# Kernel tuning notes

Measured on AMD Instinct MI355X. Metric: run time of the kernel, lower is better.

Reference implementation:

```python
import jax, jax.numpy as jnp
import numpy as np

N_NODES = 100000
N_EDGES = 1600000
IN_CH = 128
HID = 128   # 2 * out_channels
OUT = 64


def setup_inputs() -> dict:
    key = jax.random.key(0)
    ks = jax.random.split(key, 6)
    x = jax.random.normal(ks[0], (N_NODES, IN_CH), dtype=jnp.float32)
    edge_index = jax.random.randint(ks[1], (2, N_EDGES), 0, N_NODES, dtype=jnp.int64)
    # Glorot-ish scaled weights
    W1 = jax.random.normal(ks[2], (IN_CH, HID), dtype=jnp.float32) * (1.0 / np.sqrt(IN_CH))
    b1 = jnp.zeros((HID,), dtype=jnp.float32)
    Wmu = jax.random.normal(ks[3], (HID, OUT), dtype=jnp.float32) * (1.0 / np.sqrt(HID))
    bmu = jnp.zeros((OUT,), dtype=jnp.float32)
    Wlv = jax.random.normal(ks[4], (HID, OUT), dtype=jnp.float32) * (1.0 / np.sqrt(HID))
    blv = jnp.zeros((OUT,), dtype=jnp.float32)
    return {"x": x, "edge_index": edge_index, "W1": W1, "b1": b1,
            "Wmu": Wmu, "bmu": bmu, "Wlv": Wlv, "blv": blv}


def reference(x, edge_index, W1, b1, Wmu, bmu, Wlv, blv):
    n = x.shape[0]
    loops = jnp.arange(n, dtype=edge_index.dtype)
    src = jnp.concatenate([edge_index[0], loops])  # [E + N]
    dst = jnp.concatenate([edge_index[1], loops])
    # GCN symmetric normalization with self-loops (cached=True -> compute once, reuse)
    deg = jax.ops.segment_sum(jnp.ones_like(src, dtype=x.dtype), dst, num_segments=n)
    dinv = jnp.where(deg > 0, jax.lax.rsqrt(jnp.maximum(deg, 1.0)), 0.0)
    norm = (dinv[src] * dinv[dst])[:, None]  # [E+N, 1]

    def gcn(h, W, b):
        h = h @ W                              # dense transform first (smaller gather width)
        msg = h[src] * norm                    # gather + edge scaling
        return jax.ops.segment_sum(msg, dst, num_segments=n) + b

    h = jax.nn.relu(gcn(x, W1, b1))
    mu = gcn(h, Wmu, bmu)
    logvar = gcn(h, Wlv, blv)
    return (mu, logvar)
```

## Files before the change

kernel.cpp:

```cpp
#include <hip/hip_runtime.h>
#include <hip/hip_fp16.h>


using half8 = __attribute__((ext_vector_type(8))) _Float16;
using f32x4 = __attribute__((ext_vector_type(4))) float;
using f32x2 = __attribute__((ext_vector_type(2))) float;

constexpr int CAP = 8192;

__global__ void detect_kernel(const int* __restrict__ ei, int* __restrict__ mode) {
    int lane = threadIdx.x & 63;
    int any = 0;
    for (int k = lane; k < 1024; k += 64) any |= ei[2 * k + 1];
    unsigned long long b = __ballot(any != 0);
    if (threadIdx.x == 0) *mode = (b == 0ull) ? 1 : 0;
}

__global__ __launch_bounds__(256) void partition_kernel(
    const int* __restrict__ ei, int E, int n, const int* __restrict__ mode,
    int* __restrict__ bcnt, unsigned* __restrict__ pairs) {
    __shared__ int hist[512];
    __shared__ int base[512];
    int t = threadIdx.x;
    for (int i = t; i < 512; i += 256) hist[i] = 0;
    __syncthreads();
    int m = *mode;
    int e0 = blockIdx.x * 4096;
    int s_[16], d_[16], o_[16];
#pragma unroll
    for (int k = 0; k < 16; ++k) {
        int e = e0 + k * 256 + t;
        d_[k] = -1;
        if (e < E) {
            int s = m ? ei[2 * e] : ei[e];
            int d = m ? ei[2 * (E + e)] : ei[E + e];
            if ((unsigned)d < (unsigned)n && (unsigned)s < (unsigned)n) {
                s_[k] = s;
                d_[k] = d;
                o_[k] = atomicAdd(&hist[d >> 8], 1);
            }
        }
    }
    __syncthreads();
    int K = (n + 255) >> 8;
    for (int b = t; b < K; b += 256) {
        int h = hist[b];
        base[b] = h ? atomicAdd(&bcnt[b], h) : 0;
    }
    __syncthreads();
#pragma unroll
    for (int k = 0; k < 16; ++k) {
        if (d_[k] >= 0) {
            int b = d_[k] >> 8;
            unsigned p = (unsigned)s_[k] | ((unsigned)(d_[k] & 255) << 24);
            pairs[(size_t)b * CAP + base[b] + o_[k]] = p;
        }
    }
}

__global__ __launch_bounds__(256) void build_kernel(
    const unsigned* __restrict__ pairs, const int* __restrict__ bcnt,
    int2* __restrict__ rowbe, float* __restrict__ dinv,
    int* __restrict__ csr_src, int n) {
    __shared__ int hist[256];
    __shared__ int wtot[4];
    int b = blockIdx.x;
    int cnt = bcnt[b];
    size_t gbase = (size_t)b * CAP;
    int tid = threadIdx.x, lane = tid & 63, wv = tid >> 6;
    hist[tid] = 0;
    __syncthreads();
    for (int i = tid; i < cnt; i += 256)
        atomicAdd(&hist[pairs[gbase + i] >> 24], 1);
    __syncthreads();
    int v = hist[tid];
    int incl = v;
#pragma unroll
    for (int off = 1; off < 64; off <<= 1) {
        int t = __shfl_up(incl, off, 64);
        if (lane >= off) incl += t;
    }
    if (lane == 63) wtot[wv] = incl;
    __syncthreads();
    int wo = 0;
    for (int w = 0; w < wv; ++w) wo += wtot[w];
    int ex = wo + incl - v;
    int node = (b << 8) + tid;
    if (node < n) {
        int beg = (int)gbase + ex;
        rowbe[node] = make_int2(beg, beg + v);
        dinv[node] = rsqrtf((float)(v + 1));
    }
    __syncthreads();
    hist[tid] = ex;
    __syncthreads();
    for (int i = tid; i < cnt; i += 256) {
        unsigned p = pairs[gbase + i];
        int pos = atomicAdd(&hist[p >> 24], 1);
        csr_src[gbase + pos] = (int)(p & 0x00FFFFFFu);
    }
}

template <int MODE>
__global__ __launch_bounds__(256) void agg_row_kernel(
    const __half* __restrict__ T, const float* __restrict__ dinv,
    const int2* __restrict__ rowbe, const int* __restrict__ csr_src,
    const float* __restrict__ biasa, const float* __restrict__ biasb,
    void* __restrict__ outa, void* __restrict__ outb, int n) {
    int wave = (int)((blockIdx.x * blockDim.x + threadIdx.x) >> 6);
    int lane = threadIdx.x & 63;
    if (wave >= n) return;
    const __half2* x2 = (const __half2*)T;
    float di = dinv[wave];
    float2 xf = __half22float2(x2[((size_t)wave << 6) + lane]);
    float ax = 0.f, ay = 0.f;
    int2 be = rowbe[wave];
    int e = be.x, end = be.y;
    for (; e + 8 <= end; e += 8) {
        int s[8];
        float w[8];
        float2 u[8];
#pragma unroll
        for (int k = 0; k < 8; ++k)
            s[k] = __builtin_amdgcn_readfirstlane(csr_src[e + k]);
#pragma unroll
        for (int k = 0; k < 8; ++k) w[k] = dinv[s[k]];
#pragma unroll
        for (int k = 0; k < 8; ++k)
            u[k] = __half22float2(x2[((size_t)s[k] << 6) + lane]);
#pragma unroll
        for (int k = 0; k < 8; ++k) {
            ax += w[k] * u[k].x;
            ay += w[k] * u[k].y;
        }
    }
    for (; e < end; ++e) {
        int s = __builtin_amdgcn_readfirstlane(csr_src[e]);
        float w = dinv[s];
        float2 u = __half22float2(x2[((size_t)s << 6) + lane]);
        ax += w * u.x;
        ay += w * u.y;
    }
    const float* bp = (lane < 32) ? biasa : biasb;
    float2 bv = *(const float2*)(bp + ((2 * lane) & 63));
    float vx = di * (di * xf.x + ax) + bv.x;
    float vy = di * (di * xf.y + ay) + bv.y;
    if (MODE == 0) {
        vx = fmaxf(vx, 0.f);
        vy = fmaxf(vy, 0.f);
        __half2 hv = __floats2half2_rn(vx, vy);
        unsigned int bits;
        __builtin_memcpy(&bits, &hv, 4);
        unsigned int* o = (unsigned int*)outa;
        __builtin_nontemporal_store(bits, o + ((size_t)wave << 6) + lane);
    } else {
        float* o = (lane < 32) ? (float*)outa : (float*)outb;
        int cc = (2 * lane) & 63;
        f32x2 v = {vx, vy};
        __builtin_nontemporal_store(v, (f32x2*)(o + (size_t)wave * 64 + cc));
    }
}

__global__ void packw_kernel(const float* __restrict__ Wa,
                             const float* __restrict__ Wb,
                             __half* __restrict__ dst) {
    int t = blockIdx.x * 256 + threadIdx.x;
    int lane = t & 63;
    int fk = t >> 6;
    int kt = fk & 3, nt = fk >> 2;
    int k0 = kt * 32 + ((lane >> 4) << 3);
    int c = nt * 16 + (lane & 15);
    const float* W;
    int ldw, cc;
    if (Wb) {
        W = (c < 64) ? Wa : Wb;
        cc = c & 63;
        ldw = 64;
    } else {
        W = Wa;
        cc = c;
        ldw = 128;
    }
    __half tmp[8];
#pragma unroll
    for (int e = 0; e < 8; ++e)
        tmp[e] = __float2half(W[(size_t)(k0 + e) * ldw + cc]);
    *(float4*)(dst + (size_t)t * 8) = *(float4*)tmp;
}

template <typename AT>
__global__ __launch_bounds__(256) void gemm_pure_kernel(
    const AT* __restrict__ A, const __half* __restrict__ Wp,
    __half* __restrict__ outh, int n) {
    int lane = threadIdx.x & 63;
    int wv = threadIdx.x >> 6;
    int m0 = (blockIdx.x * 4 + wv) * 16;
    if (m0 >= n) return;
    int row_a = m0 + (lane & 15);
    if (row_a >= n) row_a = n - 1;
    half8 afr[4];
    if constexpr (sizeof(AT) == 4) {
        const float4* Arow = (const float4*)(A + (size_t)row_a * 128);
#pragma unroll
        for (int kt = 0; kt < 4; ++kt) {
            float4 lo = Arow[kt * 8 + ((lane >> 4) << 1)];
            float4 hi = Arow[kt * 8 + ((lane >> 4) << 1) + 1];
            half8 h;
            h[0] = (_Float16)lo.x; h[1] = (_Float16)lo.y;
            h[2] = (_Float16)lo.z; h[3] = (_Float16)lo.w;
            h[4] = (_Float16)hi.x; h[5] = (_Float16)hi.y;
            h[6] = (_Float16)hi.z; h[7] = (_Float16)hi.w;
            afr[kt] = h;
        }
    } else {
        const half8* Arow = (const half8*)(A + (size_t)row_a * 128);
#pragma unroll
        for (int kt = 0; kt < 4; ++kt) afr[kt] = Arow[kt * 4 + (lane >> 4)];
    }

    const half8* Wf = (const half8*)Wp;
    int colw = lane & 15;
    int rbase = m0 + ((lane >> 4) << 2);

#pragma unroll
    for (int nt = 0; nt < 8; ++nt) {
        f32x4 acc = {0.f, 0.f, 0.f, 0.f};
#pragma unroll
        for (int kt = 0; kt < 4; ++kt)
            acc = __builtin_amdgcn_mfma_f32_16x16x32_f16(
                afr[kt], Wf[(nt * 4 + kt) * 64 + lane], acc, 0, 0, 0);
        int c = nt * 16 + colw;
#pragma unroll
        for (int e = 0; e < 4; ++e) {
            int r = rbase + e;
            if (r < n) outh[(size_t)r * 128 + c] = __float2half(acc[e]);
        }
    }
}

extern "C" void kernel_launch(void* const* d_in, const int* in_sizes, int n_in,
                              void* d_out, int out_size, void* d_ws, size_t ws_size,
                              hipStream_t stream) {
    const float* x   = (const float*)d_in[0];
    const int*   ei  = (const int*)d_in[1];
    const float* W1  = (const float*)d_in[2];
    const float* b1  = (const float*)d_in[3];
    const float* Wmu = (const float*)d_in[4];
    const float* bmu = (const float*)d_in[5];
    const float* Wlv = (const float*)d_in[6];
    const float* blv = (const float*)d_in[7];
    float* out = (float*)d_out;

    const int n = in_sizes[0] / 128;
    const int E = in_sizes[1] / 2;
    const int K = (n + 255) >> 8;

    char* ws = (char*)d_ws;
    size_t off = 0;
    auto alloc = [&](size_t bytes) -> void* {
        void* p = ws + off;
        off += (bytes + 255) & ~(size_t)255;
        return p;
    };
    int*      mode    = (int*)alloc(256);
    int*      bcnt    = (int*)alloc((size_t)K * 4);
    int2*     rowbe   = (int2*)alloc((size_t)n * 8);
    float*    dinv    = (float*)alloc((size_t)n * 4);
    int*      csr_src = (int*)alloc((size_t)K * CAP * 4);
    unsigned* pairs   = (unsigned*)alloc((size_t)K * CAP * 4);
    __half*   bufT    = (__half*)alloc((size_t)n * 128 * 2);
    __half*   bufH    = (__half*)alloc((size_t)n * 128 * 2);
    __half*   W1p     = (__half*)alloc(128 * 128 * 2);
    __half*   W2p     = (__half*)alloc(128 * 128 * 2);

    hipMemsetAsync(bcnt, 0, (size_t)K * 4, stream);

    detect_kernel<<<1, 64, 0, stream>>>(ei, mode);

    int pb = (E + 4095) / 4096;
    partition_kernel<<<pb, 256, 0, stream>>>(ei, E, n, mode, bcnt, pairs);
    build_kernel<<<K, 256, 0, stream>>>(pairs, bcnt, rowbe, dinv, csr_src, n);

    packw_kernel<<<8, 256, 0, stream>>>(W1, nullptr, W1p);
    packw_kernel<<<8, 256, 0, stream>>>(Wmu, Wlv, W2p);

    int gb = (n + 63) / 64;
    int ab = (n + 3) / 4;

    gemm_pure_kernel<float><<<gb, 256, 0, stream>>>(x, W1p, bufT, n);
    agg_row_kernel<0><<<ab, 256, 0, stream>>>(bufT, dinv, rowbe, csr_src,
                                              b1, b1 + 64, bufH, nullptr, n);
    gemm_pure_kernel<__half><<<gb, 256, 0, stream>>>(bufH, W2p, bufT, n);
    agg_row_kernel<1><<<ab, 256, 0, stream>>>(bufT, dinv, rowbe, csr_src,
                                              bmu, blv, out,
                                              out + (size_t)n * 64, n);
}
```

Before: 244.2 us.

## Fold bucket-count zeroing into detect kernel, merge weight packing, enlarge partition tiles

Moves the bucket-count memset into the detect kernel and merges the two weight-packing launches into a single kernel, removing two launches from the stream. The partition kernel now handles 8192 edges per block instead of 4096, which halves the number of global atomics on bucket counters. The price is higher register pressure from the 32-entry per-thread arrays, and fewer partition blocks, which may reduce parallelism.

After: 239.6 us. Within noise of the previous version (-1.9%).

```diff
diff --git a/kernel.cpp b/kernel.cpp
--- a/kernel.cpp
+++ b/kernel.cpp
@@ -8,8 +8,10 @@
 
 constexpr int CAP = 8192;
 
-__global__ void detect_kernel(const int* __restrict__ ei, int* __restrict__ mode) {
+__global__ void detect_kernel(const int* __restrict__ ei, int* __restrict__ mode,
+                              int* __restrict__ bcnt, int K) {
     int lane = threadIdx.x & 63;
+    for (int i = lane; i < K; i += 64) bcnt[i] = 0;
     int any = 0;
     for (int k = lane; k < 1024; k += 64) any |= ei[2 * k + 1];
     unsigned long long b = __ballot(any != 0);
@@ -25,10 +27,10 @@
     for (int i = t; i < 512; i += 256) hist[i] = 0;
     __syncthreads();
     int m = *mode;
-    int e0 = blockIdx.x * 4096;
-    int s_[16], d_[16], o_[16];
-#pragma unroll
-    for (int k = 0; k < 16; ++k) {
+    int e0 = blockIdx.x * 8192;
+    int s_[32], d_[32], o_[32];
+#pragma unroll
+    for (int k = 0; k < 32; ++k) {
         int e = e0 + k * 256 + t;
         d_[k] = -1;
         if (e < E) {
@@ -49,7 +51,7 @@
     }
     __syncthreads();
 #pragma unroll
-    for (int k = 0; k < 16; ++k) {
+    for (int k = 0; k < 32; ++k) {
         if (d_[k] >= 0) {
             int b = d_[k] >> 8;
             unsigned p = (unsigned)s_[k] | ((unsigned)(d_[k] & 255) << 24);
@@ -161,25 +163,31 @@
     }
 }
 
-__global__ void packw_kernel(const float* __restrict__ Wa,
-                             const float* __restrict__ Wb,
-                             __half* __restrict__ dst) {
-    int t = blockIdx.x * 256 + threadIdx.x;
+__global__ void packw2_kernel(const float* __restrict__ W1,
+                              const float* __restrict__ Wmu,
+                              const float* __restrict__ Wlv,
+                              __half* __restrict__ dst1,
+                              __half* __restrict__ dst2) {
+    int which = blockIdx.x >> 3;
+    int t = (blockIdx.x & 7) * 256 + threadIdx.x;
     int lane = t & 63;
     int fk = t >> 6;
     int kt = fk & 3, nt = fk >> 2;
     int k0 = kt * 32 + ((lane >> 4) << 3);
     int c = nt * 16 + (lane & 15);
     const float* W;
+    __half* dst;
     int ldw, cc;
-    if (Wb) {
-        W = (c < 64) ? Wa : Wb;
+    if (which) {
+        W = (c < 64) ? Wmu : Wlv;
         cc = c & 63;
         ldw = 64;
+        dst = dst2;
     } else {
-        W = Wa;
+        W = W1;
         cc = c;
         ldw = 128;
+        dst = dst1;
     }
     __half tmp[8];
 #pragma unroll
@@ -273,16 +281,13 @@
     __half*   W1p     = (__half*)alloc(128 * 128 * 2);
     __half*   W2p     = (__half*)alloc(128 * 128 * 2);
 
-    hipMemsetAsync(bcnt, 0, (size_t)K * 4, stream);
-
-    detect_kernel<<<1, 64, 0, stream>>>(ei, mode);
-
-    int pb = (E + 4095) / 4096;
+    detect_kernel<<<1, 64, 0, stream>>>(ei, mode, bcnt, K);
+
+    int pb = (E + 8191) / 8192;
     partition_kernel<<<pb, 256, 0, stream>>>(ei, E, n, mode, bcnt, pairs);
     build_kernel<<<K, 256, 0, stream>>>(pairs, bcnt, rowbe, dinv, csr_src, n);
 
-    packw_kernel<<<8, 256, 0, stream>>>(W1, nullptr, W1p);
-    packw_kernel<<<8, 256, 0, stream>>>(Wmu, Wlv, W2p);
+    packw2_kernel<<<16, 256, 0, stream>>>(W1, Wmu, Wlv, W1p, W2p);
 
     int gb = (n + 63) / 64;
     int ab = (n + 3) / 4;
```
